# Kernel optimization log

Measured on AMD Instinct MI355X. Metric: run time of the kernel, lower is better.

Reference implementation:

```python
import jax, jax.numpy as jnp
import numpy as np

D_MODEL = 256
NHEAD = 8
NLAYERS = 4
DFF = 1024
PATCH = 8
INPUT = 32
C = 2
DATA_DIM = C * PATCH * PATCH  # 128
P = (INPUT // PATCH) ** 2     # 16
NEG = -1.0e6                  # _neg_large_for_dtype(float32)
EPS = 1e-5


def _ln(x, w, b):
    m = x.mean(-1, keepdims=True)
    v = ((x - m) ** 2).mean(-1, keepdims=True)
    return (x - m) / jnp.sqrt(v + EPS) * w + b


def _forward(img_baseline, acq_dts_float, nan_token, pad_embed, emb_w, emb_b, spatial_pos,
             t_w1, t_b1, t_w2, t_b2, t_w3, t_b3,
             in_proj_w, in_proj_b, out_proj_w, out_proj_b,
             lin1_w, lin1_b, lin2_w, lin2_b, norm1_w, norm1_b, norm2_w, norm2_b,
             mean_w1, mean_b1, mean_w2, mean_b2, lv_w1, lv_b1, lv_w2, lv_b2):
    B, T, Cc, Hh, Ww = img_baseline.shape
    p = PATCH
    gh, gw = Hh // p, Ww // p
    L = T * P
    frame_pad = jnp.all(img_baseline == -9999.0, axis=(2, 3, 4))  # (B,T)
    nan_pix = jnp.isnan(img_baseline)
    token = jnp.clip(nan_token, -10.0, 10.0).reshape(1, 1, Cc, 1, 1)
    x = jnp.clip(jnp.where(nan_pix, token, img_baseline), -10.0, 10.0)

    def patchify(a):  # b t c (h ph)(w pw) -> b t (h w) (c ph pw)
        return a.reshape(B, T, Cc, gh, p, gw, p).transpose(0, 1, 3, 5, 2, 4, 6).reshape(B, T, P, Cc * p * p)

    xp = patchify(x)
    seq_nan = patchify(nan_pix).all(-1).reshape(B, L)
    seq_pad = jnp.broadcast_to(frame_pad[:, :, None], (B, T, P)).reshape(B, L)

    # temporal MLP embedding
    t_in = jnp.where(jnp.isnan(acq_dts_float), 0.0, acq_dts_float)[..., None]  # (B,T,1)
    h = jax.nn.relu(t_in @ t_w1.T + t_b1)
    h = jax.nn.relu(h @ t_w2.T + t_b2)
    temb = h @ t_w3.T + t_b3  # (B,T,D)

    z = xp @ emb_w.T + emb_b + spatial_pos + temb[:, :, None, :]  # (B,T,P,D)
    z = z.reshape(B, L, D_MODEL)
    z = jnp.where(seq_pad[..., None], pad_embed, z)  # masked_scatter of pad_embed

    # additive attention mask: rows with NaN/pad patches are fully masked except diagonal
    masked_rows = seq_nan | seq_pad
    mask = jnp.broadcast_to(jnp.where(masked_rows[:, :, None], NEG, 0.0), (B, L, L))
    eye = jnp.eye(L, dtype=bool)
    mask = jnp.where(eye[None, :, :] & masked_rows[:, :, None], 0.0, mask)
    # key_padding_mask merged additively on key columns
    mask = mask + jnp.where(seq_pad[:, None, :], NEG, 0.0)
    mask = mask[:, None, :, :]  # (B,1,L,L), shared across heads

    dh = D_MODEL // NHEAD
    scale = 1.0 / np.sqrt(dh).astype(np.float32)
    for l in range(NLAYERS):
        qkv = z @ in_proj_w[l].T + in_proj_b[l]
        q, k, v = jnp.split(qkv, 3, axis=-1)
        q = q.reshape(B, L, NHEAD, dh).transpose(0, 2, 1, 3)
        k = k.reshape(B, L, NHEAD, dh).transpose(0, 2, 1, 3)
        v = v.reshape(B, L, NHEAD, dh).transpose(0, 2, 1, 3)
        scores = jnp.einsum('bhqd,bhkd->bhqk', q, k) * scale + mask
        attn = jax.nn.softmax(scores, axis=-1)
        o = jnp.einsum('bhqk,bhkd->bhqd', attn, v).transpose(0, 2, 1, 3).reshape(B, L, D_MODEL)
        o = o @ out_proj_w[l].T + out_proj_b[l]
        z = _ln(z + o, norm1_w[l], norm1_b[l])
        ff = jax.nn.relu(z @ lin1_w[l].T + lin1_b[l]) @ lin2_w[l].T + lin2_b[l]
        z = _ln(z + ff, norm2_w[l], norm2_b[l])

    mean = jnp.clip(jax.nn.relu(z @ mean_w1.T + mean_b1) @ mean_w2.T + mean_b2, -10.0, 10.0)
    logvar = jnp.clip(jax.nn.relu(z @ lv_w1.T + lv_b1) @ lv_w2.T + lv_b2, -10.0, 5.0)

    def unpatch(a):  # b t (h w)(c ph pw) -> b t c (h ph)(w pw)
        return a.reshape(B, T, gh, gw, Cc, p, p).transpose(0, 1, 4, 2, 5, 3, 6).reshape(B, T, Cc, Hh, Ww)

    mean = unpatch(mean.reshape(B, T, P, DATA_DIM))
    logvar = unpatch(logvar.reshape(B, T, P, DATA_DIM))
    return mean[:, -1], logvar[:, -1]


def setup_inputs() -> dict:
    key = jax.random.key(0)
    ks = iter(jax.random.split(key, 48))

    def rn(shape, scale=0.02):
        return jax.random.normal(next(ks), shape, dtype=jnp.float32) * scale

    B, T = 4, 64
    z = lambda s: jnp.zeros(s, jnp.float32)
    return {
        'img_baseline': jax.random.normal(next(ks), (B, T, C, INPUT, INPUT), dtype=jnp.float32),
        'acq_dts_float': jax.random.uniform(next(ks), (B, T), dtype=jnp.float32) * 3000.0,
        'nan_token': rn((C,)),
        'pad_embed': rn((1, 1, D_MODEL)),
        'emb_w': rn((D_MODEL, DATA_DIM)),
        'emb_b': z((D_MODEL,)),
        'spatial_pos': rn((1, 1, P, D_MODEL)),
        't_w1': rn((64, 1)), 't_b1': z((64,)),
        't_w2': rn((128, 64)), 't_b2': z((128,)),
        't_w3': rn((D_MODEL, 128)), 't_b3': z((D_MODEL,)),
        'in_proj_w': rn((NLAYERS, 3 * D_MODEL, D_MODEL)),
        'in_proj_b': z((NLAYERS, 3 * D_MODEL)),
        'out_proj_w': rn((NLAYERS, D_MODEL, D_MODEL)),
        'out_proj_b': z((NLAYERS, D_MODEL)),
        'lin1_w': rn((NLAYERS, DFF, D_MODEL)), 'lin1_b': z((NLAYERS, DFF)),
        'lin2_w': rn((NLAYERS, D_MODEL, DFF)), 'lin2_b': z((NLAYERS, D_MODEL)),
        'norm1_w': jnp.ones((NLAYERS, D_MODEL), jnp.float32), 'norm1_b': z((NLAYERS, D_MODEL)),
        'norm2_w': jnp.ones((NLAYERS, D_MODEL), jnp.float32), 'norm2_b': z((NLAYERS, D_MODEL)),
        'mean_w1': rn((DFF, D_MODEL)), 'mean_b1': z((DFF,)),
        'mean_w2': rn((DATA_DIM, DFF)), 'mean_b2': z((DATA_DIM,)),
        'lv_w1': rn((DFF, D_MODEL)), 'lv_b1': z((DFF,)),
        'lv_w2': rn((DATA_DIM, DFF)), 'lv_b2': z((DATA_DIM,)),
    }


def reference(img_baseline, acq_dts_float, nan_token, pad_embed, emb_w, emb_b, spatial_pos,
              t_w1, t_b1, t_w2, t_b2, t_w3, t_b3,
              in_proj_w, in_proj_b, out_proj_w, out_proj_b,
              lin1_w, lin1_b, lin2_w, lin2_b, norm1_w, norm1_b, norm2_w, norm2_b,
              mean_w1, mean_b1, mean_w2, mean_b2, lv_w1, lv_b1, lv_w2, lv_b2):
    return _forward(img_baseline, acq_dts_float, nan_token, pad_embed, emb_w, emb_b, spatial_pos,
                    t_w1, t_b1, t_w2, t_b2, t_w3, t_b3,
                    in_proj_w, in_proj_b, out_proj_w, out_proj_b,
                    lin1_w, lin1_b, lin2_w, lin2_b, norm1_w, norm1_b, norm2_w, norm2_b,
                    mean_w1, mean_b1, mean_w2, mean_b2, lv_w1, lv_b1, lv_w2, lv_b2)
```

## Files before the change

### kernel.cpp

```cpp
#include <hip/hip_runtime.h>
#include <hip/hip_bf16.h>

#define D_MODEL 256
#define NHEAD 8
#define DH 32
#define NLAYERS 4
#define DFF 1024
#define CC 2
#define DATA_DIM 128
#define PP 16
#define TT 64
#define BB 4
#define LL 1024
#define NEGV -1000000.0f

typedef __bf16 bf16_t;
typedef __bf16 bf16x8 __attribute__((ext_vector_type(8)));
typedef __bf16 bf16x4 __attribute__((ext_vector_type(4)));
typedef float v4f __attribute__((ext_vector_type(4)));

__device__ __forceinline__ bool my_isnan(float v) {
    unsigned u = __float_as_uint(v);
    return (u & 0x7fffffffu) > 0x7f800000u;
}

__device__ __forceinline__ void gld16(bf16_t* l, const bf16_t* g) {
    __builtin_amdgcn_global_load_lds(
        (const __attribute__((address_space(1))) void*)g,
        (__attribute__((address_space(3))) void*)l, 16, 0, 0);
}

__global__ void f2b_all_kernel(const float* __restrict__ s0, bf16_t* __restrict__ d0, int n0,
                               const float* __restrict__ s1, bf16_t* __restrict__ d1, int n1,
                               const float* __restrict__ s2, bf16_t* __restrict__ d2, int n2,
                               const float* __restrict__ s3, bf16_t* __restrict__ d3, int n3,
                               const float* __restrict__ s4, bf16_t* __restrict__ d4, int n4,
                               const float* __restrict__ s5, bf16_t* __restrict__ d5, int n5,
                               const float* __restrict__ s6, bf16_t* __restrict__ d6, int n6,
                               const float* __restrict__ s7, bf16_t* __restrict__ d7, int n7,
                               const float* __restrict__ s8, bf16_t* __restrict__ d8, int n8) {
    int i = (blockIdx.x * 256 + threadIdx.x) * 4;
    const float* s;
    bf16_t* d;
    if (i < n0) { s = s0; d = d0; }
    else if ((i -= n0) < n1) { s = s1; d = d1; }
    else if ((i -= n1) < n2) { s = s2; d = d2; }
    else if ((i -= n2) < n3) { s = s3; d = d3; }
    else if ((i -= n3) < n4) { s = s4; d = d4; }
    else if ((i -= n4) < n5) { s = s5; d = d5; }
    else if ((i -= n5) < n6) { s = s6; d = d6; }
    else if ((i -= n6) < n7) { s = s7; d = d7; }
    else if ((i -= n7) < n8) { s = s8; d = d8; }
    else return;
    float4 v = *(const float4*)(s + i);
    bf16x4 o = {(bf16_t)v.x, (bf16_t)v.y, (bf16_t)v.z, (bf16_t)v.w};
    *(bf16x4*)(d + i) = o;
}

__global__ void prep_frame_kernel(const float* __restrict__ img,
                                  const float* __restrict__ acq,
                                  const float* __restrict__ t_w1, const float* __restrict__ t_b1,
                                  const float* __restrict__ t_w2, const float* __restrict__ t_b2,
                                  const float* __restrict__ t_w3, const float* __restrict__ t_b3,
                                  float* __restrict__ temb, int* __restrict__ framepad) {
    int f = blockIdx.x;
    int tid = threadIdx.x;
    __shared__ float h1[64];
    __shared__ float h2[128];
    __shared__ int sAll;
    if (tid == 0) sAll = 1;
    __syncthreads();
    const float* fr = img + (size_t)f * (CC * 32 * 32);
    bool allpad = true;
    #pragma unroll
    for (int i = 0; i < 8; ++i) {
        float v = fr[tid + i * 256];
        allpad = allpad && (v == -9999.0f);
    }
    if (!allpad) sAll = 0;
    __syncthreads();
    if (tid == 0) framepad[f] = sAll;

    float t_in = acq[f];
    if (my_isnan(t_in)) t_in = 0.0f;
    if (tid < 64) h1[tid] = fmaxf(t_w1[tid] * t_in + t_b1[tid], 0.0f);
    __syncthreads();
    if (tid < 128) {
        float a = t_b2[tid];
        #pragma unroll 8
        for (int j = 0; j < 64; ++j) a += t_w2[tid * 64 + j] * h1[j];
        h2[tid] = fmaxf(a, 0.0f);
    }
    __syncthreads();
    {
        float a = t_b3[tid];
        #pragma unroll 8
        for (int j = 0; j < 128; ++j) a += t_w3[tid * 128 + j] * h2[j];
        temb[(size_t)f * D_MODEL + tid] = a;
    }
}

__global__ __launch_bounds__(256) void patchify_kernel(
    const float* __restrict__ img, const float* __restrict__ nan_token,
    const int* __restrict__ framepad,
    bf16_t* __restrict__ xpb, int* __restrict__ masked_rows,
    float* __restrict__ kmaskf) {
    int tid = threadIdx.x;
    int token = blockIdx.x * 2 + (tid >> 7);
    int dd = tid & 127;
    int l = token & 1023, b = token >> 10;
    int t = l >> 4, p = l & 15;
    int c = dd >> 6, pr = (dd >> 3) & 7, pc = dd & 7;
    int hh = (p >> 2) * 8 + pr, ww = (p & 3) * 8 + pc;
    float v = img[(((size_t)(b * TT + t) * CC + c) * 32 + hh) * 32 + ww];
    bool nanp = my_isnan(v);
    if (nanp) v = fminf(fmaxf(nan_token[c], -10.0f), 10.0f);
    v = fminf(fmaxf(v, -10.0f), 10.0f);
    xpb[(size_t)token * DATA_DIM + dd] = (bf16_t)v;

    __shared__ int wAll[4];
    unsigned long long bal = __ballot(nanp);
    if ((tid & 63) == 0) wAll[tid >> 6] = (bal == 0xFFFFFFFFFFFFFFFFull) ? 1 : 0;
    __syncthreads();
    if (tid < 2) {
        int tk = blockIdx.x * 2 + tid;
        int allnan = wAll[tid * 2] & wAll[tid * 2 + 1];
        int fp = framepad[tk >> 4];
        masked_rows[tk] = allnan | fp;
        kmaskf[tk] = fp ? NEGV : 0.0f;
    }
}

__global__ __launch_bounds__(256) void embed_gemm(
    const bf16_t* __restrict__ X, const bf16_t* __restrict__ W,
    const float* __restrict__ emb_b, const float* __restrict__ spatial,
    const float* __restrict__ temb, const float* __restrict__ pad_embed,
    const int* __restrict__ framepad,
    bf16_t* __restrict__ zb) {
    __shared__ __align__(16) bf16_t Xs[2][128 * 64];
    __shared__ __align__(16) bf16_t Ws[2][64 * 64];
    int tid = threadIdx.x;
    int wave = tid >> 6, lane = tid & 63;
    int quad = lane >> 4, l16 = lane & 15;
    int m0 = blockIdx.y * 128, n0 = blockIdx.x * 64;
    const int K = DATA_DIM, N = D_MODEL;

    v4f acc[2][4];
    #pragma unroll
    for (int i = 0; i < 2; ++i)
        #pragma unroll
        for (int j = 0; j < 4; ++j) acc[i][j] = (v4f){0.f, 0.f, 0.f, 0.f};

    int sr = tid >> 3, ss = tid & 7;
    int gc = (ss ^ (sr & 7)) * 8;

#define ESTAGE(bufi, k0)                                                          \
    do {                                                                          \
        _Pragma("unroll")                                                         \
        for (int p = 0; p < 4; ++p) {                                             \
            int r = sr + p * 32;                                                  \
            gld16(Xs[bufi] + r * 64 + ss * 8, X + (size_t)(m0 + r) * K + (k0) + gc); \
        }                                                                         \
        _Pragma("unroll")                                                         \
        for (int p = 0; p < 2; ++p) {                                             \
            int r = sr + p * 32;                                                  \
            gld16(Ws[bufi] + r * 64 + ss * 8, W + (size_t)(n0 + r) * K + (k0) + gc); \
        }                                                                         \
    } while (0)

    ESTAGE(0, 0);
    __syncthreads();
    const int T = K / 64;
    int swl = l16 & 7;
    for (int t = 0; t < T; ++t) {
        int buf = t & 1;
        if (t + 1 < T) ESTAGE(buf ^ 1, (t + 1) * 64);
        const bf16_t* Xc = Xs[buf];
        const bf16_t* Wc = Ws[buf];
        int ra = wave * 32 + l16;
        #pragma unroll
        for (int h = 0; h < 2; ++h) {
            int g8 = ((h * 4 + quad) ^ swl) * 8;
            bf16x8 af0 = *(const bf16x8*)(Xc + ra * 64 + g8);
            bf16x8 af1 = *(const bf16x8*)(Xc + (ra + 16) * 64 + g8);
            #pragma unroll
            for (int nt = 0; nt < 4; ++nt) {
                bf16x8 bfr = *(const bf16x8*)(Wc + (nt * 16 + l16) * 64 + g8);
                acc[0][nt] = __builtin_amdgcn_mfma_f32_16x16x32_bf16(af0, bfr, acc[0][nt], 0, 0, 0);
                acc[1][nt] = __builtin_amdgcn_mfma_f32_16x16x32_bf16(af1, bfr, acc[1][nt], 0, 0, 0);
            }
        }
        __syncthreads();
    }
#undef ESTAGE

    #pragma unroll
    for (int mt = 0; mt < 2; ++mt)
        #pragma unroll
        for (int nt = 0; nt < 4; ++nt) {
            int col = n0 + nt * 16 + l16;
            #pragma unroll
            for (int reg = 0; reg < 4; ++reg) {
                int row = m0 + wave * 32 + mt * 16 + quad * 4 + reg;
                int frame = row >> 4, p = row & 15;
                float v;
                if (framepad[frame]) {
                    v = pad_embed[col];
                } else {
                    v = acc[mt][nt][reg] + emb_b[col] + spatial[p * N + col]
                      + temb[(size_t)frame * N + col];
                }
                zb[(size_t)row * N + col] = (bf16_t)v;
            }
        }
}

template <int MODE, int RELU>
__global__ __launch_bounds__(256) void gemm_mfma(
    const bf16_t* __restrict__ X, const bf16_t* __restrict__ W,
    const float* __restrict__ bias, bf16_t* __restrict__ Y,
    bf16_t* __restrict__ Vt, int M, int N, int K) {
    __shared__ __align__(16) bf16_t Xs[2][128 * 64];
    __shared__ __align__(16) bf16_t Ws[2][64 * 64];
    int tid = threadIdx.x;
    int wave = tid >> 6, lane = tid & 63;
    int quad = lane >> 4, l16 = lane & 15;
    int m0 = blockIdx.y * 128, n0 = blockIdx.x * 64;

    v4f acc[2][4];
    #pragma unroll
    for (int i = 0; i < 2; ++i)
        #pragma unroll
        for (int j = 0; j < 4; ++j) acc[i][j] = (v4f){0.f, 0.f, 0.f, 0.f};

    int sr = tid >> 3, ss = tid & 7;
    int gc = (ss ^ (sr & 7)) * 8;

#define GSTAGE(bufi, k0)                                                          \
    do {                                                                          \
        _Pragma("unroll")                                                         \
        for (int p = 0; p < 4; ++p) {                                             \
            int r = sr + p * 32;                                                  \
            gld16(Xs[bufi] + r * 64 + ss * 8, X + (size_t)(m0 + r) * K + (k0) + gc); \
        }                                                                         \
        _Pragma("unroll")                                                         \
        for (int p = 0; p < 2; ++p) {                                             \
            int r = sr + p * 32;                                                  \
            gld16(Ws[bufi] + r * 64 + ss * 8, W + (size_t)(n0 + r) * K + (k0) + gc); \
        }                                                                         \
    } while (0)

    GSTAGE(0, 0);
    __syncthreads();
    const int T = K >> 6;
    int swl = l16 & 7;
    for (int t = 0; t < T; ++t) {
        int buf = t & 1;
        if (t + 1 < T) GSTAGE(buf ^ 1, (t + 1) * 64);
        const bf16_t* Xc = Xs[buf];
        const bf16_t* Wc = Ws[buf];
        int ra = wave * 32 + l16;
        #pragma unroll
        for (int h = 0; h < 2; ++h) {
            int g8 = ((h * 4 + quad) ^ swl) * 8;
            bf16x8 af0 = *(const bf16x8*)(Xc + ra * 64 + g8);
            bf16x8 af1 = *(const bf16x8*)(Xc + (ra + 16) * 64 + g8);
            #pragma unroll
            for (int nt = 0; nt < 4; ++nt) {
                bf16x8 bfr = *(const bf16x8*)(Wc + (nt * 16 + l16) * 64 + g8);
                acc[0][nt] = __builtin_amdgcn_mfma_f32_16x16x32_bf16(af0, bfr, acc[0][nt], 0, 0, 0);
                acc[1][nt] = __builtin_amdgcn_mfma_f32_16x16x32_bf16(af1, bfr, acc[1][nt], 0, 0, 0);
            }
        }
        __syncthreads();
    }
#undef GSTAGE

    if constexpr (MODE == 1) {
        #pragma unroll
        for (int mt = 0; mt < 2; ++mt)
            #pragma unroll
            for (int nt = 0; nt < 4; ++nt) {
                int col = n0 + nt * 16 + l16;
                float bv = bias[col];
                #pragma unroll
                for (int reg = 0; reg < 4; ++reg) {
                    int row = m0 + wave * 32 + mt * 16 + quad * 4 + reg;
                    float v = acc[mt][nt][reg] + bv;
                    if (RELU) v = fmaxf(v, 0.0f);
                    Y[(size_t)row * N + col] = (bf16_t)v;
                }
            }
    } else {
        if (n0 < 512) {
            #pragma unroll
            for (int mt = 0; mt < 2; ++mt)
                #pragma unroll
                for (int nt = 0; nt < 4; ++nt) {
                    int col = n0 + nt * 16 + l16;
                    float bv = bias[col];
                    #pragma unroll
                    for (int reg = 0; reg < 4; ++reg) {
                        int row = m0 + wave * 32 + mt * 16 + quad * 4 + reg;
                        float v = acc[mt][nt][reg] + bv;
                        Y[(size_t)row * 768 + col] = (bf16_t)v;
                    }
                }
        } else {
            bf16_t* VT = &Xs[0][0];
            #pragma unroll
            for (int mt = 0; mt < 2; ++mt)
                #pragma unroll
                for (int nt = 0; nt < 4; ++nt) {
                    int cl = nt * 16 + l16;
                    float bv = bias[n0 + cl];
                    #pragma unroll
                    for (int reg = 0; reg < 4; ++reg) {
                        int rl = wave * 32 + mt * 16 + quad * 4 + reg;
                        VT[cl * 136 + rl] = (bf16_t)(acc[mt][nt][reg] + bv);
                    }
                }
            __syncthreads();
            int b = m0 >> 10, l0m = m0 & 1023;
            int cl = tid >> 2;
            int rbase = (tid & 3) * 8;
            int cg = n0 + cl - 512;
            int h = cg >> 5, d = cg & 31;
            bf16_t* dst = Vt + (((size_t)(b * NHEAD + h)) * DH + d) * LL + l0m;
            #pragma unroll
            for (int u = 0; u < 4; ++u)
                *(uint4*)(dst + rbase + u * 32) = *(const uint4*)(VT + cl * 136 + rbase + u * 32);
        }
    }
}

__global__ __launch_bounds__(256) void gemm_small(
    const bf16_t* __restrict__ X, const bf16_t* __restrict__ W,
    const float* __restrict__ bias, const bf16_t* __restrict__ Zres,
    bf16_t* __restrict__ Y, int M, int N, int K) {
    __shared__ __align__(16) bf16_t Xs[2][64 * 64];
    __shared__ __align__(16) bf16_t Ws[2][64 * 64];
    int tid = threadIdx.x;
    int wave = tid >> 6, lane = tid & 63;
    int quad = lane >> 4, l16 = lane & 15;
    int m0 = blockIdx.y * 64, n0 = blockIdx.x * 64;

    v4f acc[4];
    #pragma unroll
    for (int j = 0; j < 4; ++j) acc[j] = (v4f){0.f, 0.f, 0.f, 0.f};

    int sr = tid >> 3, ss = tid & 7;
    int gc = (ss ^ (sr & 7)) * 8;

#define SSTAGE(bufi, k0)                                                          \
    do {                                                                          \
        _Pragma("unroll")                                                         \
        for (int p = 0; p < 2; ++p) {                                             \
            int r = sr + p * 32;                                                  \
            gld16(Xs[bufi] + r * 64 + ss * 8, X + (size_t)(m0 + r) * K + (k0) + gc); \
            gld16(Ws[bufi] + r * 64 + ss * 8, W + (size_t)(n0 + r) * K + (k0) + gc); \
        }                                                                         \
    } while (0)

    SSTAGE(0, 0);
    __syncthreads();
    const int T = K >> 6;
    int swl = l16 & 7;
    for (int t = 0; t < T; ++t) {
        int buf = t & 1;
        if (t + 1 < T) SSTAGE(buf ^ 1, (t + 1) * 64);
        const bf16_t* Xc = Xs[buf];
        const bf16_t* Wc = Ws[buf];
        int ra = wave * 16 + l16;
        #pragma unroll
        for (int h = 0; h < 2; ++h) {
            int g8 = ((h * 4 + quad) ^ swl) * 8;
            bf16x8 af = *(const bf16x8*)(Xc + ra * 64 + g8);
            #pragma unroll
            for (int nt = 0; nt < 4; ++nt) {
                bf16x8 bfr = *(const bf16x8*)(Wc + (nt * 16 + l16) * 64 + g8);
                acc[nt] = __builtin_amdgcn_mfma_f32_16x16x32_bf16(af, bfr, acc[nt], 0, 0, 0);
            }
        }
        __syncthreads();
    }
#undef SSTAGE

    #pragma unroll
    for (int nt = 0; nt < 4; ++nt) {
        int col = n0 + nt * 16 + l16;
        float bv = bias[col];
        #pragma unroll
        for (int reg = 0; reg < 4; ++reg) {
            int row = m0 + wave * 16 + quad * 4 + reg;
            float r = acc[nt][reg] + bv + (float)Zres[(size_t)row * N + col];
            Y[(size_t)row * N + col] = (bf16_t)r;
        }
    }
}

__global__ __launch_bounds__(256) void attn_mfma(
    const bf16_t* __restrict__ qkvb, const bf16_t* __restrict__ Vt,
    const int* __restrict__ masked_rows, const float* __restrict__ kmaskf,
    bf16_t* __restrict__ Ob) {
    __shared__ __align__(16) bf16_t Ks[2][128 * 40];
    __shared__ __align__(16) bf16_t Vs[2][32 * 136];
    __shared__ __align__(16) float  Kms[2][128];
    __shared__ __align__(16) bf16_t Ps[4][16 * 136];

    int tid = threadIdx.x;
    int wave = tid >> 6, lane = tid & 63;
    int quad = lane >> 4, l16 = lane & 15;
    int bid = blockIdx.x;
    int h = bid & 7, b = (bid >> 3) & 3, qt = bid >> 5;
    int q0 = qt * 64 + wave * 16;
    const float scale = 0.17677669529663687f;

    bf16x8 qf = *(const bf16x8*)(qkvb + ((size_t)(b * LL) + q0 + l16) * 768 + h * DH + quad * 8);

    int mq = masked_rows[b * LL + q0 + l16];
    int qg = q0 + l16;

    float lrun = 0.0f;
    v4f oacc[2];
    oacc[0] = (v4f){0.f, 0.f, 0.f, 0.f};
    oacc[1] = (v4f){0.f, 0.f, 0.f, 0.f};

    int kr = tid >> 1, kh = (tid & 1) * 16;
    int vd = tid >> 3, vs0 = (tid & 7) * 8;
    const bf16_t* Kbase = qkvb + (size_t)(b * LL) * 768 + 256 + h * DH;
    const bf16_t* Vbase = Vt + (((size_t)(b * NHEAD + h)) * DH) * LL;
    const float* kmbase = kmaskf + b * LL;

    uint4 ka, kb, va, vb;
    float kmg;
    #define LOADC(c)                                                            \
        do {                                                                    \
            int _k0 = (c) * 128;                                                \
            ka = *(const uint4*)(Kbase + (size_t)(_k0 + kr) * 768 + kh);        \
            kb = *(const uint4*)(Kbase + (size_t)(_k0 + kr) * 768 + kh + 8);    \
            va = *(const uint4*)(Vbase + (size_t)vd * LL + _k0 + vs0);          \
            vb = *(const uint4*)(Vbase + (size_t)vd * LL + _k0 + 64 + vs0);     \
            kmg = (tid < 128) ? kmbase[_k0 + tid] : 0.0f;                       \
        } while (0)
    #define WRITEBUF(buf)                                                       \
        do {                                                                    \
            *(uint4*)(Ks[(buf)] + kr * 40 + kh) = ka;                           \
            *(uint4*)(Ks[(buf)] + kr * 40 + kh + 8) = kb;                       \
            *(uint4*)(Vs[(buf)] + vd * 136 + vs0) = va;                         \
            *(uint4*)(Vs[(buf)] + vd * 136 + 64 + vs0) = vb;                    \
            if (tid < 128) Kms[(buf)][tid] = kmg;                               \
        } while (0)

    LOADC(0);
    WRITEBUF(0);
    LOADC(1);

    bf16_t* Pw = Ps[wave];
    for (int c = 0; c < 8; ++c) {
        __syncthreads();
        int cur = c & 1;
        if (c + 1 < 8) WRITEBUF(cur ^ 1);
        if (c + 2 < 8) LOADC(c + 2);

        int k0 = c * 128;
        const bf16_t* Kc = Ks[cur];
        const bf16_t* Vc = Vs[cur];
        const float* kmc = Kms[cur];

        v4f sf[8];
        #pragma unroll
        for (int nt = 0; nt < 8; ++nt) {
            bf16x8 kf = *(const bf16x8*)(Kc + (nt * 16 + l16) * 40 + quad * 8);
            v4f zf = (v4f){0.f, 0.f, 0.f, 0.f};
            sf[nt] = __builtin_amdgcn_mfma_f32_16x16x32_bf16(kf, qf, zf, 0, 0, 0);
        }

        #pragma unroll
        for (int nt = 0; nt < 8; ++nt) {
            int kbase_nt = k0 + nt * 16 + quad * 4;
            float4 kmv = *(const float4*)(kmc + nt * 16 + quad * 4);
            float pv[4];
            #pragma unroll
            for (int reg = 0; reg < 4; ++reg) {
                float km = (reg == 0) ? kmv.x : (reg == 1) ? kmv.y : (reg == 2) ? kmv.z : kmv.w;
                float v = sf[nt][reg] * scale + km;
                if (mq && (qg != kbase_nt + reg)) v += NEGV;
                float p = __expf(v);
                lrun += p;
                pv[reg] = p;
            }
            bf16x4 pp = {(bf16_t)pv[0], (bf16_t)pv[1], (bf16_t)pv[2], (bf16_t)pv[3]};
            *(bf16x4*)(Pw + l16 * 136 + nt * 16 + quad * 4) = pp;
        }

        #pragma unroll
        for (int kt = 0; kt < 4; ++kt) {
            bf16x8 pf = *(const bf16x8*)(Pw + l16 * 136 + kt * 32 + quad * 8);
            #pragma unroll
            for (int nt2 = 0; nt2 < 2; ++nt2) {
                bf16x8 vf = *(const bf16x8*)(Vc + (nt2 * 16 + l16) * 136 + kt * 32 + quad * 8);
                oacc[nt2] = __builtin_amdgcn_mfma_f32_16x16x32_bf16(pf, vf, oacc[nt2], 0, 0, 0);
            }
        }
    }
    #undef LOADC
    #undef WRITEBUF

    lrun += __shfl_xor(lrun, 16);
    lrun += __shfl_xor(lrun, 32);
    float lq[4];
    #pragma unroll
    for (int reg = 0; reg < 4; ++reg) lq[reg] = __shfl(lrun, quad * 4 + reg);

    #pragma unroll
    for (int nt2 = 0; nt2 < 2; ++nt2)
        #pragma unroll
        for (int reg = 0; reg < 4; ++reg) {
            size_t row = (size_t)(b * LL) + q0 + quad * 4 + reg;
            Ob[row * 256 + h * DH + nt2 * 16 + l16] = (bf16_t)(oacc[nt2][reg] / lq[reg]);
        }
}

__global__ __launch_bounds__(256) void ln_kernel(
    const bf16_t* __restrict__ tmps, const float* __restrict__ w,
    const float* __restrict__ b, bf16_t* __restrict__ zb) {
    int wave = threadIdx.x >> 6, lane = threadIdx.x & 63;
    int row = blockIdx.x * 4 + wave;
    bf16x4 xb = *(const bf16x4*)(tmps + (size_t)row * D_MODEL + lane * 4);
    float x0 = (float)xb[0], x1 = (float)xb[1], x2 = (float)xb[2], x3 = (float)xb[3];
    float s = x0 + x1 + x2 + x3;
    #pragma unroll
    for (int off = 32; off > 0; off >>= 1) s += __shfl_xor(s, off);
    float mean = s * (1.0f / D_MODEL);
    float dx0 = x0 - mean, dx1 = x1 - mean, dx2 = x2 - mean, dx3 = x3 - mean;
    float sq = dx0 * dx0 + dx1 * dx1 + dx2 * dx2 + dx3 * dx3;
    #pragma unroll
    for (int off = 32; off > 0; off >>= 1) sq += __shfl_xor(sq, off);
    float inv = 1.0f / sqrtf(sq * (1.0f / D_MODEL) + 1e-5f);
    float4 wv = ((const float4*)w)[lane];
    float4 bv = ((const float4*)b)[lane];
    bf16x4 rb = {(bf16_t)(dx0 * inv * wv.x + bv.x),
                 (bf16_t)(dx1 * inv * wv.y + bv.y),
                 (bf16_t)(dx2 * inv * wv.z + bv.z),
                 (bf16_t)(dx3 * inv * wv.w + bv.w)};
    *(bf16x4*)(zb + (size_t)row * D_MODEL + lane * 4) = rb;
}

__global__ __launch_bounds__(256) void head_h_kernel(
    const bf16_t* __restrict__ zb, const bf16_t* __restrict__ W1b,
    const float* __restrict__ mean_b1, const float* __restrict__ lv_b1,
    bf16_t* __restrict__ hb) {
    __shared__ __align__(16) bf16_t Xs[2][64 * 64];
    __shared__ __align__(16) bf16_t Ws[2][64 * 64];
    int tid = threadIdx.x;
    int wave = tid >> 6, lane = tid & 63;
    int quad = lane >> 4, l16 = lane & 15;
    int head = blockIdx.y;
    int n0 = blockIdx.x * 64;
    const bf16_t* W1h = W1b + (size_t)head * DFF * D_MODEL;
    const float* B1f = head ? lv_b1 : mean_b1;
    bf16_t* hbh = hb + (size_t)head * 64 * DFF;

    v4f acc[4];
    #pragma unroll
    for (int j = 0; j < 4; ++j) acc[j] = (v4f){0.f, 0.f, 0.f, 0.f};

    int sr = tid >> 3, ss = tid & 7;
    int gc = (ss ^ (sr & 7)) * 8;

#define HSTAGE(bufi, k0)                                                          \
    do {                                                                          \
        _Pragma("unroll")                                                         \
        for (int p = 0; p < 2; ++p) {                                             \
            int r = sr + p * 32;                                                  \
            const bf16_t* xr = zb + (size_t)((r >> 4) * LL + (TT - 1) * PP + (r & 15)) * D_MODEL; \
            gld16(Xs[bufi] + r * 64 + ss * 8, xr + (k0) + gc);                    \
            gld16(Ws[bufi] + r * 64 + ss * 8, W1h + (size_t)(n0 + r) * D_MODEL + (k0) + gc); \
        }                                                                         \
    } while (0)

    HSTAGE(0, 0);
    __syncthreads();
    const int T = D_MODEL / 64;
    int swl = l16 & 7;
    for (int t = 0; t < T; ++t) {
        int buf = t & 1;
        if (t + 1 < T) HSTAGE(buf ^ 1, (t + 1) * 64);
        const bf16_t* Xc = Xs[buf];
        const bf16_t* Wc = Ws[buf];
        int ra = wave * 16 + l16;
        #pragma unroll
        for (int h = 0; h < 2; ++h) {
            int g8 = ((h * 4 + quad) ^ swl) * 8;
            bf16x8 af = *(const bf16x8*)(Xc + ra * 64 + g8);
            #pragma unroll
            for (int nt = 0; nt < 4; ++nt) {
                bf16x8 bfr = *(const bf16x8*)(Wc + (nt * 16 + l16) * 64 + g8);
                acc[nt] = __builtin_amdgcn_mfma_f32_16x16x32_bf16(af, bfr, acc[nt], 0, 0, 0);
            }
        }
        __syncthreads();
    }
#undef HSTAGE

    #pragma unroll
    for (int nt = 0; nt < 4; ++nt) {
        int col = n0 + nt * 16 + l16;
        float bv = B1f[col];
        #pragma unroll
        for (int reg = 0; reg < 4; ++reg) {
            int row = wave * 16 + quad * 4 + reg;
            hbh[(size_t)row * DFF + col] = (bf16_t)fmaxf(acc[nt][reg] + bv, 0.0f);
        }
    }
}

__global__ __launch_bounds__(256) void head_out_kernel(
    const bf16_t* __restrict__ hb, const bf16_t* __restrict__ W2b,
    const float* __restrict__ mean_b2, const float* __restrict__ lv_b2,
    float* __restrict__ out) {
    __shared__ __align__(16) bf16_t hrow[DFF];
    int tid = threadIdx.x;
    int bid = blockIdx.x;
    int head = bid >> 7, rr = (bid >> 1) & 63, half = bid & 1;
    int b = rr >> 4, p = rr & 15;

    if (tid < 128)
        *(uint4*)(hrow + tid * 8) =
            *(const uint4*)(hb + ((size_t)head * 64 + rr) * DFF + tid * 8);
    __syncthreads();

    int ol = tid >> 2, quarter = tid & 3;
    int o = half * 64 + ol;
    const bf16_t* wrow = W2b + ((size_t)head * DATA_DIM + o) * DFF + quarter * 256;
    const bf16_t* hseg = hrow + quarter * 256;
    float acc = 0.0f;
    #pragma unroll 8
    for (int j = 0; j < 32; ++j) {
        bf16x8 w = *(const bf16x8*)(wrow + j * 8);
        bf16x8 hv = *(const bf16x8*)(hseg + j * 8);
        #pragma unroll
        for (int e = 0; e < 8; ++e) acc += (float)w[e] * (float)hv[e];
    }
    acc += __shfl_xor(acc, 1);
    acc += __shfl_xor(acc, 2);
    if (quarter == 0) {
        const float* B2 = head ? lv_b2 : mean_b2;
        float hi = head ? 5.0f : 10.0f;
        float v = fminf(fmaxf(acc + B2[o], -10.0f), hi);
        int c = o >> 6;
        int pr = (o >> 3) & 7, pc = o & 7;
        int hh = (p >> 2) * 8 + pr, ww = (p & 3) * 8 + pc;
        out[(size_t)head * 8192 + ((size_t)(b * CC + c)) * 1024 + hh * 32 + ww] = v;
    }
}

extern "C" void kernel_launch(void* const* d_in, const int* in_sizes, int n_in,
                              void* d_out, int out_size, void* d_ws, size_t ws_size,
                              hipStream_t stream) {
    const float* img        = (const float*)d_in[0];
    const float* acq        = (const float*)d_in[1];
    const float* nan_token  = (const float*)d_in[2];
    const float* pad_embed  = (const float*)d_in[3];
    const float* emb_w      = (const float*)d_in[4];
    const float* emb_b      = (const float*)d_in[5];
    const float* spatial    = (const float*)d_in[6];
    const float* t_w1       = (const float*)d_in[7];
    const float* t_b1       = (const float*)d_in[8];
    const float* t_w2       = (const float*)d_in[9];
    const float* t_b2       = (const float*)d_in[10];
    const float* t_w3       = (const float*)d_in[11];
    const float* t_b3       = (const float*)d_in[12];
    const float* in_proj_w  = (const float*)d_in[13];
    const float* in_proj_b  = (const float*)d_in[14];
    const float* out_proj_w = (const float*)d_in[15];
    const float* out_proj_b = (const float*)d_in[16];
    const float* lin1_w     = (const float*)d_in[17];
    const float* lin1_b     = (const float*)d_in[18];
    const float* lin2_w     = (const float*)d_in[19];
    const float* lin2_b     = (const float*)d_in[20];
    const float* norm1_w    = (const float*)d_in[21];
    const float* norm1_b    = (const float*)d_in[22];
    const float* norm2_w    = (const float*)d_in[23];
    const float* norm2_b    = (const float*)d_in[24];
    const float* mean_w1    = (const float*)d_in[25];
    const float* mean_b1    = (const float*)d_in[26];
    const float* mean_w2    = (const float*)d_in[27];
    const float* mean_b2    = (const float*)d_in[28];
    const float* lv_w1      = (const float*)d_in[29];
    const float* lv_b1      = (const float*)d_in[30];
    const float* lv_w2      = (const float*)d_in[31];
    const float* lv_b2      = (const float*)d_in[32];

    const int M = BB * LL;

    char* wsb = (char*)d_ws;
    float* temb    = (float*)wsb;                    wsb += (size_t)BB * TT * D_MODEL * 4;
    float* kmaskf  = (float*)wsb;                    wsb += M * 4;
    int* framepad  = (int*)wsb;                      wsb += BB * TT * 4;
    int* masked    = (int*)wsb;                      wsb += M * 4;
    wsb = (char*)(((uintptr_t)wsb + 255) & ~(uintptr_t)255);
    bf16_t* zb     = (bf16_t*)wsb;                   wsb += (size_t)M * D_MODEL * 2;
    bf16_t* tmps   = (bf16_t*)wsb;                   wsb += (size_t)M * D_MODEL * 2;
    bf16_t* xpb    = (bf16_t*)wsb;                   wsb += (size_t)M * DATA_DIM * 2;
    bf16_t* qkvb   = (bf16_t*)wsb;                   wsb += (size_t)M * 768 * 2;
    bf16_t* VtG    = (bf16_t*)wsb;                   wsb += (size_t)M * D_MODEL * 2;
    bf16_t* attnb  = (bf16_t*)wsb;                   wsb += (size_t)M * D_MODEL * 2;
    bf16_t* ff1b   = (bf16_t*)wsb;                   wsb += (size_t)M * DFF * 2;
    bf16_t* inb    = (bf16_t*)wsb;                   wsb += (size_t)NLAYERS * 768 * D_MODEL * 2;
    bf16_t* outb   = (bf16_t*)wsb;                   wsb += (size_t)NLAYERS * D_MODEL * D_MODEL * 2;
    bf16_t* l1b    = (bf16_t*)wsb;                   wsb += (size_t)NLAYERS * DFF * D_MODEL * 2;
    bf16_t* l2b    = (bf16_t*)wsb;                   wsb += (size_t)NLAYERS * D_MODEL * DFF * 2;
    bf16_t* embwb  = (bf16_t*)wsb;                   wsb += (size_t)D_MODEL * DATA_DIM * 2;
    bf16_t* w1b    = (bf16_t*)wsb;                   wsb += (size_t)2 * DFF * D_MODEL * 2;
    bf16_t* w2b    = (bf16_t*)wsb;                   wsb += (size_t)2 * DATA_DIM * DFF * 2;
    bf16_t* hb     = (bf16_t*)wsb;                   wsb += (size_t)2 * 64 * DFF * 2;

    float* outF = (float*)d_out;

    {
        int n1 = NLAYERS * 768 * D_MODEL;
        int n2 = NLAYERS * D_MODEL * D_MODEL;
        int n3 = NLAYERS * DFF * D_MODEL;
        int n4 = NLAYERS * D_MODEL * DFF;
        int n5 = D_MODEL * DATA_DIM;
        int n6 = DFF * D_MODEL;
        int n7 = DFF * D_MODEL;
        int n8 = DATA_DIM * DFF;
        int n9 = DATA_DIM * DFF;
        int tot = n1 + n2 + n3 + n4 + n5 + n6 + n7 + n8 + n9;
        f2b_all_kernel<<<(tot / 4 + 255) / 256, 256, 0, stream>>>(
            in_proj_w, inb, n1, out_proj_w, outb, n2, lin1_w, l1b, n3,
            lin2_w, l2b, n4, emb_w, embwb, n5,
            mean_w1, w1b, n6, lv_w1, w1b + (size_t)DFF * D_MODEL, n7,
            mean_w2, w2b, n8, lv_w2, w2b + (size_t)DATA_DIM * DFF, n9);
    }

    prep_frame_kernel<<<BB * TT, 256, 0, stream>>>(img, acq, t_w1, t_b1, t_w2, t_b2,
                                                   t_w3, t_b3, temb, framepad);
    patchify_kernel<<<M / 2, 256, 0, stream>>>(img, nan_token, framepad, xpb, masked, kmaskf);
    embed_gemm<<<dim3(D_MODEL / 64, M / 128), 256, 0, stream>>>(
        xpb, embwb, emb_b, spatial, temb, pad_embed, framepad, zb);

    for (int l = 0; l < NLAYERS; ++l) {
        gemm_mfma<2, 0><<<dim3(768 / 64, M / 128), 256, 0, stream>>>(
            zb, inb + (size_t)l * 768 * D_MODEL, in_proj_b + (size_t)l * 768,
            qkvb, VtG, M, 768, D_MODEL);
        attn_mfma<<<BB * NHEAD * (LL / 64), 256, 0, stream>>>(qkvb, VtG, masked, kmaskf, attnb);
        gemm_small<<<dim3(D_MODEL / 64, M / 64), 256, 0, stream>>>(
            attnb, outb + (size_t)l * D_MODEL * D_MODEL, out_proj_b + (size_t)l * D_MODEL,
            zb, tmps, M, D_MODEL, D_MODEL);
        ln_kernel<<<M / 4, 256, 0, stream>>>(tmps, norm1_w + l * D_MODEL,
                                             norm1_b + l * D_MODEL, zb);
        gemm_mfma<1, 1><<<dim3(DFF / 64, M / 128), 256, 0, stream>>>(
            zb, l1b + (size_t)l * DFF * D_MODEL, lin1_b + (size_t)l * DFF,
            ff1b, nullptr, M, DFF, D_MODEL);
        gemm_small<<<dim3(D_MODEL / 64, M / 64), 256, 0, stream>>>(
            ff1b, l2b + (size_t)l * D_MODEL * DFF, lin2_b + (size_t)l * D_MODEL,
            zb, tmps, M, D_MODEL, DFF);
        ln_kernel<<<M / 4, 256, 0, stream>>>(tmps, norm2_w + l * D_MODEL,
                                             norm2_b + l * D_MODEL, zb);
    }

    head_h_kernel<<<dim3(DFF / 64, 2), 256, 0, stream>>>(zb, w1b, mean_b1, lv_b1, hb);
    head_out_kernel<<<256, 256, 0, stream>>>(hb, w2b, mean_b2, lv_b2, outF);
}
```

Before: 396.1 us.

## Fuse residual LayerNorm into full-row output GEMMs and merge prep kernels

Replaces the 64x64-tile out-proj and FFN2 GEMMs plus the separate LayerNorm kernel with one kernel per block that computes a full 256-column row tile. Row statistics are reduced across lanes with shuffles and the normalized result is written in place to zb. This removes the tmps round trip and 8 launches per forward. The weight-conversion and frame-prep kernels are also merged into one launch. In exchange, the fused GEMM grid shrinks to M/64 blocks, and the larger per-block W staging plus the 16 accumulators per lane may reduce occupancy.

Result: slower. 440.4 us (+11.2%).

```diff
diff --git a/kernel.cpp b/kernel.cpp
--- a/kernel.cpp
+++ b/kernel.cpp
@@ -30,41 +30,48 @@
         (__attribute__((address_space(3))) void*)l, 16, 0, 0);
 }
 
-__global__ void f2b_all_kernel(const float* __restrict__ s0, bf16_t* __restrict__ d0, int n0,
-                               const float* __restrict__ s1, bf16_t* __restrict__ d1, int n1,
-                               const float* __restrict__ s2, bf16_t* __restrict__ d2, int n2,
-                               const float* __restrict__ s3, bf16_t* __restrict__ d3, int n3,
-                               const float* __restrict__ s4, bf16_t* __restrict__ d4, int n4,
-                               const float* __restrict__ s5, bf16_t* __restrict__ d5, int n5,
-                               const float* __restrict__ s6, bf16_t* __restrict__ d6, int n6,
-                               const float* __restrict__ s7, bf16_t* __restrict__ d7, int n7,
-                               const float* __restrict__ s8, bf16_t* __restrict__ d8, int n8) {
-    int i = (blockIdx.x * 256 + threadIdx.x) * 4;
-    const float* s;
-    bf16_t* d;
-    if (i < n0) { s = s0; d = d0; }
-    else if ((i -= n0) < n1) { s = s1; d = d1; }
-    else if ((i -= n1) < n2) { s = s2; d = d2; }
-    else if ((i -= n2) < n3) { s = s3; d = d3; }
-    else if ((i -= n3) < n4) { s = s4; d = d4; }
-    else if ((i -= n4) < n5) { s = s5; d = d5; }
-    else if ((i -= n5) < n6) { s = s6; d = d6; }
-    else if ((i -= n6) < n7) { s = s7; d = d7; }
-    else if ((i -= n7) < n8) { s = s8; d = d8; }
-    else return;
-    float4 v = *(const float4*)(s + i);
-    bf16x4 o = {(bf16_t)v.x, (bf16_t)v.y, (bf16_t)v.z, (bf16_t)v.w};
-    *(bf16x4*)(d + i) = o;
-}
-
-__global__ void prep_frame_kernel(const float* __restrict__ img,
-                                  const float* __restrict__ acq,
-                                  const float* __restrict__ t_w1, const float* __restrict__ t_b1,
-                                  const float* __restrict__ t_w2, const float* __restrict__ t_b2,
-                                  const float* __restrict__ t_w3, const float* __restrict__ t_b3,
-                                  float* __restrict__ temb, int* __restrict__ framepad) {
+__global__ __launch_bounds__(256) void f2b_prep_kernel(
+    const float* __restrict__ in_proj_w, bf16_t* __restrict__ inb,
+    const float* __restrict__ out_proj_w, bf16_t* __restrict__ outb,
+    const float* __restrict__ lin1_w, bf16_t* __restrict__ l1b,
+    const float* __restrict__ lin2_w, bf16_t* __restrict__ l2b,
+    const float* __restrict__ emb_w, bf16_t* __restrict__ embwb,
+    const float* __restrict__ mean_w1, const float* __restrict__ lv_w1, bf16_t* __restrict__ w1b,
+    const float* __restrict__ mean_w2, const float* __restrict__ lv_w2, bf16_t* __restrict__ w2b,
+    const float* __restrict__ img, const float* __restrict__ acq,
+    const float* __restrict__ t_w1, const float* __restrict__ t_b1,
+    const float* __restrict__ t_w2, const float* __restrict__ t_b2,
+    const float* __restrict__ t_w3, const float* __restrict__ t_b3,
+    float* __restrict__ temb, int* __restrict__ framepad) {
+    const int n0 = NLAYERS * 768 * D_MODEL;
+    const int n1 = NLAYERS * D_MODEL * D_MODEL;
+    const int n2 = NLAYERS * DFF * D_MODEL;
+    const int n3 = NLAYERS * D_MODEL * DFF;
+    const int n4 = D_MODEL * DATA_DIM;
+    const int n5 = DFF * D_MODEL;
+    const int n6 = DFF * D_MODEL;
+    const int n7 = DATA_DIM * DFF;
+    const int n8 = DATA_DIM * DFF;
+    int tid = threadIdx.x;
+    int i = (blockIdx.x * 256 + tid) * 4;
+    const float* s = nullptr; bf16_t* d = nullptr;
+    if (i < n0) { s = in_proj_w; d = inb; }
+    else if ((i -= n0) < n1) { s = out_proj_w; d = outb; }
+    else if ((i -= n1) < n2) { s = lin1_w; d = l1b; }
+    else if ((i -= n2) < n3) { s = lin2_w; d = l2b; }
+    else if ((i -= n3) < n4) { s = emb_w; d = embwb; }
+    else if ((i -= n4) < n5) { s = mean_w1; d = w1b; }
+    else if ((i -= n5) < n6) { s = lv_w1; d = w1b + n5; }
+    else if ((i -= n6) < n7) { s = mean_w2; d = w2b; }
+    else if ((i -= n7) < n8) { s = lv_w2; d = w2b + n7; }
+    if (s) {
+        float4 v = *(const float4*)(s + i);
+        bf16x4 o = {(bf16_t)v.x, (bf16_t)v.y, (bf16_t)v.z, (bf16_t)v.w};
+        *(bf16x4*)(d + i) = o;
+    }
+
+    if (blockIdx.x >= BB * TT) return;
     int f = blockIdx.x;
-    int tid = threadIdx.x;
     __shared__ float h1[64];
     __shared__ float h2[128];
     __shared__ int sAll;
@@ -73,8 +80,8 @@
     const float* fr = img + (size_t)f * (CC * 32 * 32);
     bool allpad = true;
     #pragma unroll
-    for (int i = 0; i < 8; ++i) {
-        float v = fr[tid + i * 256];
+    for (int k = 0; k < 8; ++k) {
+        float v = fr[tid + k * 256];
         allpad = allpad && (v == -9999.0f);
     }
     if (!allpad) sAll = 0;
@@ -324,8 +331,8 @@
             int b = m0 >> 10, l0m = m0 & 1023;
             int cl = tid >> 2;
             int rbase = (tid & 3) * 8;
-            int cg = n0 + cl - 512;
-            int h = cg >> 5, d = cg & 31;
+            int cg2 = n0 + cl - 512;
+            int h = cg2 >> 5, d = cg2 & 31;
             bf16_t* dst = Vt + (((size_t)(b * NHEAD + h)) * DH + d) * LL + l0m;
             #pragma unroll
             for (int u = 0; u < 4; ++u)
@@ -334,41 +341,46 @@
     }
 }
 
-__global__ __launch_bounds__(256) void gemm_small(
+__global__ __launch_bounds__(256) void gemm_row_ln(
     const bf16_t* __restrict__ X, const bf16_t* __restrict__ W,
     const float* __restrict__ bias, const bf16_t* __restrict__ Zres,
-    bf16_t* __restrict__ Y, int M, int N, int K) {
+    bf16_t* __restrict__ Y, const float* __restrict__ lnw,
+    const float* __restrict__ lnb, int K) {
     __shared__ __align__(16) bf16_t Xs[2][64 * 64];
-    __shared__ __align__(16) bf16_t Ws[2][64 * 64];
+    __shared__ __align__(16) bf16_t Ws[2][256 * 64];
     int tid = threadIdx.x;
     int wave = tid >> 6, lane = tid & 63;
     int quad = lane >> 4, l16 = lane & 15;
-    int m0 = blockIdx.y * 64, n0 = blockIdx.x * 64;
-
-    v4f acc[4];
-    #pragma unroll
-    for (int j = 0; j < 4; ++j) acc[j] = (v4f){0.f, 0.f, 0.f, 0.f};
+    int m0 = blockIdx.x * 64;
+
+    v4f acc[16];
+    #pragma unroll
+    for (int j = 0; j < 16; ++j) acc[j] = (v4f){0.f, 0.f, 0.f, 0.f};
 
     int sr = tid >> 3, ss = tid & 7;
     int gc = (ss ^ (sr & 7)) * 8;
 
-#define SSTAGE(bufi, k0)                                                          \
+#define RSTAGE(bufi, k0)                                                          \
     do {                                                                          \
         _Pragma("unroll")                                                         \
         for (int p = 0; p < 2; ++p) {                                             \
             int r = sr + p * 32;                                                  \
             gld16(Xs[bufi] + r * 64 + ss * 8, X + (size_t)(m0 + r) * K + (k0) + gc); \
-            gld16(Ws[bufi] + r * 64 + ss * 8, W + (size_t)(n0 + r) * K + (k0) + gc); \
+        }                                                                         \
+        _Pragma("unroll")                                                         \
+        for (int p = 0; p < 8; ++p) {                                             \
+            int r = sr + p * 32;                                                  \
+            gld16(Ws[bufi] + r * 64 + ss * 8, W + (size_t)r * K + (k0) + gc);     \
         }                                                                         \
     } while (0)
 
-    SSTAGE(0, 0);
+    RSTAGE(0, 0);
     __syncthreads();
     const int T = K >> 6;
     int swl = l16 & 7;
     for (int t = 0; t < T; ++t) {
         int buf = t & 1;
-        if (t + 1 < T) SSTAGE(buf ^ 1, (t + 1) * 64);
+        if (t + 1 < T) RSTAGE(buf ^ 1, (t + 1) * 64);
         const bf16_t* Xc = Xs[buf];
         const bf16_t* Wc = Ws[buf];
         int ra = wave * 16 + l16;
@@ -377,24 +389,48 @@
             int g8 = ((h * 4 + quad) ^ swl) * 8;
             bf16x8 af = *(const bf16x8*)(Xc + ra * 64 + g8);
             #pragma unroll
-            for (int nt = 0; nt < 4; ++nt) {
+            for (int nt = 0; nt < 16; ++nt) {
                 bf16x8 bfr = *(const bf16x8*)(Wc + (nt * 16 + l16) * 64 + g8);
                 acc[nt] = __builtin_amdgcn_mfma_f32_16x16x32_bf16(af, bfr, acc[nt], 0, 0, 0);
             }
         }
         __syncthreads();
     }
-#undef SSTAGE
-
-    #pragma unroll
-    for (int nt = 0; nt < 4; ++nt) {
-        int col = n0 + nt * 16 + l16;
+#undef RSTAGE
+
+    float wv[16], bvv[16];
+    #pragma unroll
+    for (int nt = 0; nt < 16; ++nt) {
+        int col = nt * 16 + l16;
         float bv = bias[col];
+        wv[nt] = lnw[col];
+        bvv[nt] = lnb[col];
         #pragma unroll
         for (int reg = 0; reg < 4; ++reg) {
             int row = m0 + wave * 16 + quad * 4 + reg;
-            float r = acc[nt][reg] + bv + (float)Zres[(size_t)row * N + col];
-            Y[(size_t)row * N + col] = (bf16_t)r;
+            acc[nt][reg] += bv + (float)Zres[(size_t)row * D_MODEL + col];
+        }
+    }
+    #pragma unroll
+    for (int reg = 0; reg < 4; ++reg) {
+        float s = 0.0f;
+        #pragma unroll
+        for (int nt = 0; nt < 16; ++nt) s += acc[nt][reg];
+        s += __shfl_xor(s, 1); s += __shfl_xor(s, 2);
+        s += __shfl_xor(s, 4); s += __shfl_xor(s, 8);
+        float mean = s * (1.0f / D_MODEL);
+        float sq = 0.0f;
+        #pragma unroll
+        for (int nt = 0; nt < 16; ++nt) { float d = acc[nt][reg] - mean; sq += d * d; }
+        sq += __shfl_xor(sq, 1); sq += __shfl_xor(sq, 2);
+        sq += __shfl_xor(sq, 4); sq += __shfl_xor(sq, 8);
+        float inv = 1.0f / sqrtf(sq * (1.0f / D_MODEL) + 1e-5f);
+        int row = m0 + wave * 16 + quad * 4 + reg;
+        #pragma unroll
+        for (int nt = 0; nt < 16; ++nt) {
+            int col = nt * 16 + l16;
+            Y[(size_t)row * D_MODEL + col] =
+                (bf16_t)((acc[nt][reg] - mean) * inv * wv[nt] + bvv[nt]);
         }
     }
 }
@@ -520,31 +556,6 @@
             size_t row = (size_t)(b * LL) + q0 + quad * 4 + reg;
             Ob[row * 256 + h * DH + nt2 * 16 + l16] = (bf16_t)(oacc[nt2][reg] / lq[reg]);
         }
-}
-
-__global__ __launch_bounds__(256) void ln_kernel(
-    const bf16_t* __restrict__ tmps, const float* __restrict__ w,
-    const float* __restrict__ b, bf16_t* __restrict__ zb) {
-    int wave = threadIdx.x >> 6, lane = threadIdx.x & 63;
-    int row = blockIdx.x * 4 + wave;
-    bf16x4 xb = *(const bf16x4*)(tmps + (size_t)row * D_MODEL + lane * 4);
-    float x0 = (float)xb[0], x1 = (float)xb[1], x2 = (float)xb[2], x3 = (float)xb[3];
-    float s = x0 + x1 + x2 + x3;
-    #pragma unroll
-    for (int off = 32; off > 0; off >>= 1) s += __shfl_xor(s, off);
-    float mean = s * (1.0f / D_MODEL);
-    float dx0 = x0 - mean, dx1 = x1 - mean, dx2 = x2 - mean, dx3 = x3 - mean;
-    float sq = dx0 * dx0 + dx1 * dx1 + dx2 * dx2 + dx3 * dx3;
-    #pragma unroll
-    for (int off = 32; off > 0; off >>= 1) sq += __shfl_xor(sq, off);
-    float inv = 1.0f / sqrtf(sq * (1.0f / D_MODEL) + 1e-5f);
-    float4 wv = ((const float4*)w)[lane];
-    float4 bv = ((const float4*)b)[lane];
-    bf16x4 rb = {(bf16_t)(dx0 * inv * wv.x + bv.x),
-                 (bf16_t)(dx1 * inv * wv.y + bv.y),
-                 (bf16_t)(dx2 * inv * wv.z + bv.z),
-                 (bf16_t)(dx3 * inv * wv.w + bv.w)};
-    *(bf16x4*)(zb + (size_t)row * D_MODEL + lane * 4) = rb;
 }
 
 __global__ __launch_bounds__(256) void head_h_kernel(
@@ -702,7 +713,6 @@
     int* masked    = (int*)wsb;                      wsb += M * 4;
     wsb = (char*)(((uintptr_t)wsb + 255) & ~(uintptr_t)255);
     bf16_t* zb     = (bf16_t*)wsb;                   wsb += (size_t)M * D_MODEL * 2;
-    bf16_t* tmps   = (bf16_t*)wsb;                   wsb += (size_t)M * D_MODEL * 2;
     bf16_t* xpb    = (bf16_t*)wsb;                   wsb += (size_t)M * DATA_DIM * 2;
     bf16_t* qkvb   = (bf16_t*)wsb;                   wsb += (size_t)M * 768 * 2;
     bf16_t* VtG    = (bf16_t*)wsb;                   wsb += (size_t)M * D_MODEL * 2;
@@ -720,25 +730,15 @@
     float* outF = (float*)d_out;
 
     {
-        int n1 = NLAYERS * 768 * D_MODEL;
-        int n2 = NLAYERS * D_MODEL * D_MODEL;
-        int n3 = NLAYERS * DFF * D_MODEL;
-        int n4 = NLAYERS * D_MODEL * DFF;
-        int n5 = D_MODEL * DATA_DIM;
-        int n6 = DFF * D_MODEL;
-        int n7 = DFF * D_MODEL;
-        int n8 = DATA_DIM * DFF;
-        int n9 = DATA_DIM * DFF;
-        int tot = n1 + n2 + n3 + n4 + n5 + n6 + n7 + n8 + n9;
-        f2b_all_kernel<<<(tot / 4 + 255) / 256, 256, 0, stream>>>(
-            in_proj_w, inb, n1, out_proj_w, outb, n2, lin1_w, l1b, n3,
-            lin2_w, l2b, n4, emb_w, embwb, n5,
-            mean_w1, w1b, n6, lv_w1, w1b + (size_t)DFF * D_MODEL, n7,
-            mean_w2, w2b, n8, lv_w2, w2b + (size_t)DATA_DIM * DFF, n9);
-    }
-
-    prep_frame_kernel<<<BB * TT, 256, 0, stream>>>(img, acq, t_w1, t_b1, t_w2, t_b2,
-                                                   t_w3, t_b3, temb, framepad);
+        int tot = NLAYERS * 768 * D_MODEL + NLAYERS * D_MODEL * D_MODEL +
+                  NLAYERS * DFF * D_MODEL + NLAYERS * D_MODEL * DFF +
+                  D_MODEL * DATA_DIM + 2 * DFF * D_MODEL + 2 * DATA_DIM * DFF;
+        f2b_prep_kernel<<<(tot / 4 + 255) / 256, 256, 0, stream>>>(
+            in_proj_w, inb, out_proj_w, outb, lin1_w, l1b, lin2_w, l2b,
+            emb_w, embwb, mean_w1, lv_w1, w1b, mean_w2, lv_w2, w2b,
+            img, acq, t_w1, t_b1, t_w2, t_b2, t_w3, t_b3, temb, framepad);
+    }
+
     patchify_kernel<<<M / 2, 256, 0, stream>>>(img, nan_token, framepad, xpb, masked, kmaskf);
     embed_gemm<<<dim3(D_MODEL / 64, M / 128), 256, 0, stream>>>(
         xpb, embwb, emb_b, spatial, temb, pad_embed, framepad, zb);
@@ -748,19 +748,15 @@
             zb, inb + (size_t)l * 768 * D_MODEL, in_proj_b + (size_t)l * 768,
             qkvb, VtG, M, 768, D_MODEL);
         attn_mfma<<<BB * NHEAD * (LL / 64), 256, 0, stream>>>(qkvb, VtG, masked, kmaskf, attnb);
-        gemm_small<<<dim3(D_MODEL / 64, M / 64), 256, 0, stream>>>(
+        gemm_row_ln<<<M / 64, 256, 0, stream>>>(
             attnb, outb + (size_t)l * D_MODEL * D_MODEL, out_proj_b + (size_t)l * D_MODEL,
-            zb, tmps, M, D_MODEL, D_MODEL);
-        ln_kernel<<<M / 4, 256, 0, stream>>>(tmps, norm1_w + l * D_MODEL,
-                                             norm1_b + l * D_MODEL, zb);
+            zb, zb, norm1_w + l * D_MODEL, norm1_b + l * D_MODEL, D_MODEL);
         gemm_mfma<1, 1><<<dim3(DFF / 64, M / 128), 256, 0, stream>>>(
             zb, l1b + (size_t)l * DFF * D_MODEL, lin1_b + (size_t)l * DFF,
             ff1b, nullptr, M, DFF, D_MODEL);
-        gemm_small<<<dim3(D_MODEL / 64, M / 64), 256, 0, stream>>>(
+        gemm_row_ln<<<M / 64, 256, 0, stream>>>(
             ff1b, l2b + (size_t)l * D_MODEL * DFF, lin2_b + (size_t)l * D_MODEL,
-            zb, tmps, M, D_MODEL, DFF);
-        ln_kernel<<<M / 4, 256, 0, stream>>>(tmps, norm2_w + l * D_MODEL,
-                                             norm2_b + l * D_MODEL, zb);
+            zb, zb, norm2_w + l * D_MODEL, norm2_b + l * D_MODEL, DFF);
     }
 
     head_h_kernel<<<dim3(DFF / 64, 2), 256, 0, stream>>>(zb, w1b, mean_b1, lv_b1, hb);
```
